# Kernel tuning notes

Measured on AMD Instinct MI355X. Metric: run time of the kernel, lower is better.

Reference implementation:

```python
import jax, jax.numpy as jnp
import numpy as np
import math

B, T, D, H = 4, 2048, 1024, 16
HD = D // H  # head dim = 64

def setup_inputs() -> dict:
    key = jax.random.key(0)
    ks = jax.random.split(key, 4)
    scale = 1.0 / math.sqrt(D)
    return {
        "x": jax.random.normal(ks[0], (B, T, D), dtype=jnp.float32),
        "Wq": jax.random.normal(ks[1], (D, D), dtype=jnp.float32) * scale,
        "bq": jnp.zeros((D,), dtype=jnp.float32),
        "Wk": jax.random.normal(ks[2], (D, D), dtype=jnp.float32) * scale,
        "bk": jnp.zeros((D,), dtype=jnp.float32),
        "Wv": jax.random.normal(ks[3], (D, D), dtype=jnp.float32) * scale,
        "bv": jnp.zeros((D,), dtype=jnp.float32),
    }

def reference(x, Wq, bq, Wk, bk, Wv, bv):
    b, t, d = x.shape
    # QKV projections (nn.Dense): x @ W + b
    q = x @ Wq + bq
    k = x @ Wk + bk
    v = x @ Wv + bv
    # b n (h d) -> b h n d
    def split_heads(y):
        return y.reshape(b, t, H, HD).transpose(0, 2, 1, 3)
    q, k, v = split_heads(q), split_heads(k), split_heads(v)
    # scaled dot-product attention; scale by sqrt(features // heads)
    scores = jnp.einsum("bhqd,bhkd->bhqk", q, k) / math.sqrt(HD)
    attn = jax.nn.softmax(scores, axis=-1)
    # dropout rate 0.0 / eval mode => identity
    out = jnp.einsum("bhqk,bhkd->bhqd", attn, v)
    # b h n d -> b n (h d)
    return out.transpose(0, 2, 1, 3).reshape(b, t, d)
```

## Files before the change

### kernel.cpp

```cpp
#include <hip/hip_runtime.h>
#include <math.h>

typedef unsigned short u16;
typedef short short8 __attribute__((ext_vector_type(8)));
typedef u16 u16x4 __attribute__((ext_vector_type(4)));
typedef float f32x4 __attribute__((ext_vector_type(4)));
typedef __bf16 bf16x8 __attribute__((ext_vector_type(8)));

#define B_ 4
#define T_ 2048
#define D_ 1024
#define H_ 16
#define HD_ 64
#define BT_ 8192

__device__ __forceinline__ u16 f2bf(float f) {
  unsigned u = __builtin_bit_cast(unsigned, f);
  u = u + 0x7fffu + ((u >> 16) & 1u);
  return (u16)(u >> 16);
}
__device__ __forceinline__ f32x4 mfma16(short8 a, short8 b, f32x4 c) {
  return __builtin_amdgcn_mfma_f32_16x16x32_bf16(
      __builtin_bit_cast(bf16x8, a), __builtin_bit_cast(bf16x8, b), c, 0, 0, 0);
}
__device__ __forceinline__ void async16(u16* lds, const u16* g) {
  __builtin_amdgcn_global_load_lds(
      (const __attribute__((address_space(1))) unsigned int*)g,
      (__attribute__((address_space(3))) unsigned int*)lds, 16, 0, 0);
}

__global__ __launch_bounds__(256) void prep(
    const float* __restrict__ x, const float* __restrict__ Wq,
    const float* __restrict__ Wk, const float* __restrict__ Wv,
    u16* __restrict__ xbf, u16* __restrict__ wtq, u16* __restrict__ wtk,
    u16* __restrict__ wtv) {
  __shared__ float sh[32][33];
  if (blockIdx.y < 256) {
    int bid = blockIdx.y * 32 + blockIdx.x;
    int i = (bid * 256 + threadIdx.x) * 4;
    float4 v = *(const float4*)&x[i];
    u16x4 o = {f2bf(v.x), f2bf(v.y), f2bf(v.z), f2bf(v.w)};
    *(u16x4*)&xbf[i] = o;
    return;
  }
  const int yy = blockIdx.y - 256;
  const int wsel = yy >> 5;
  const float* in = (wsel == 0) ? Wq : (wsel == 1) ? Wk : Wv;
  u16* out = (wsel == 0) ? wtq : (wsel == 1) ? wtk : wtv;
  const int bx = blockIdx.x * 32, by = (yy & 31) * 32;
  const int col = threadIdx.x & 31, r8 = threadIdx.x >> 5;
#pragma unroll
  for (int i = 0; i < 4; i++) {
    int row = r8 + i * 8;
    sh[row][col] = in[(size_t)(by + row) * 1024 + bx + col];
  }
  __syncthreads();
#pragma unroll
  for (int i = 0; i < 4; i++) {
    int row = r8 + i * 8;
    out[(size_t)(bx + row) * 1024 + by + col] = f2bf(sh[col][row]);
  }
}

__global__ __launch_bounds__(512, 2) void gemm_qkv3(
    const u16* __restrict__ xbf, const u16* __restrict__ wtq,
    const u16* __restrict__ wtk, const u16* __restrict__ wtv,
    const float* __restrict__ bq, const float* __restrict__ bk,
    const float* __restrict__ bv, u16* __restrict__ qh, u16* __restrict__ kh,
    u16* __restrict__ vth, float qscale) {
  extern __shared__ __align__(16) u16 smem[];
  u16* As = smem;
  u16* Bs = smem + 32768;

  const int proj = blockIdx.y >> 2;
  const int fy = blockIdx.y & 3;
  const u16* Rm;
  const u16* Cm;
  const float* bias;
  u16* out;
  float scale;
  int r0, c0, vmode;
  if (proj == 0) {
    Rm = wtq; Cm = xbf; bias = bq; out = qh; scale = qscale; vmode = 0;
    r0 = fy * 256; c0 = blockIdx.x * 256;
  } else if (proj == 1) {
    Rm = wtk; Cm = xbf; bias = bk; out = kh; scale = 1.0f; vmode = 0;
    r0 = fy * 256; c0 = blockIdx.x * 256;
  } else {
    Rm = xbf; Cm = wtv; bias = bv; out = vth; scale = 1.0f; vmode = 1;
    r0 = blockIdx.x * 256; c0 = fy * 256;
  }
  const int tid = threadIdx.x;
  const int lane = tid & 63;
  const int w = tid >> 6;
  const int wr = w >> 2, wc = w & 3;
  const int c = lane & 15, q4 = lane >> 4;
  const int cx7 = c & 7;
  const int sr = tid >> 3, pc = tid & 7;
  const int scx = (pc ^ (sr & 7)) * 8;
  const int k0o = (q4 ^ cx7) * 8;
  const int k1o = ((4 + q4) ^ cx7) * 8;
  const int brow0 = (wc & 1) * 64;

  f32x4 acc[8][4];
#pragma unroll
  for (int i = 0; i < 8; i++)
#pragma unroll
    for (int j = 0; j < 4; j++) {
      f32x4 z = {0.f, 0.f, 0.f, 0.f};
      acc[i][j] = z;
    }

#define STAGE_A(n, h)                                                        \
  {                                                                          \
    const u16* s_ = Rm + (size_t)(r0 + (h)*128 + sr) * 1024 + (n)*64 + scx;  \
    u16* d_ = As + ((((n)&1) * 2 + (h)) * 8192) + tid * 8;                   \
    async16(d_, s_);                                                         \
    async16(d_ + 4096, s_ + (size_t)64 * 1024);                              \
  }
#define STAGE_B(n, h)                                                        \
  {                                                                          \
    const u16* s_ = Cm + (size_t)(c0 + (h)*128 + sr) * 1024 + (n)*64 + scx;  \
    u16* d_ = Bs + ((((n)&1) * 2 + (h)) * 8192) + tid * 8;                   \
    async16(d_, s_);                                                         \
    async16(d_ + 4096, s_ + (size_t)64 * 1024);                              \
  }

  STAGE_B(0, 0); STAGE_A(0, 0); STAGE_B(0, 1); STAGE_A(0, 1);
  STAGE_B(1, 0); STAGE_A(1, 0);
  asm volatile("s_waitcnt vmcnt(4)" ::: "memory");
  asm volatile("s_barrier" ::: "memory");

#pragma unroll 2
  for (int n = 0; n < 16; ++n) {
    const u16* Aslot = As + (((n & 1) * 2 + wr) * 8192);
    const u16* Bslot = Bs + (((n & 1) * 2 + (wc >> 1)) * 8192);
    short8 aF[4][2], bF[4][2];

#pragma unroll
    for (int ii = 0; ii < 4; ii++) {
      aF[ii][0] = *(const short8*)&Aslot[(ii * 16 + c) * 64 + k0o];
      aF[ii][1] = *(const short8*)&Aslot[(ii * 16 + c) * 64 + k1o];
    }
#pragma unroll
    for (int jj = 0; jj < 2; jj++) {
      bF[jj][0] = *(const short8*)&Bslot[(brow0 + jj * 16 + c) * 64 + k0o];
      bF[jj][1] = *(const short8*)&Bslot[(brow0 + jj * 16 + c) * 64 + k1o];
    }
    STAGE_B((n + 1) & 15, 1);
    asm volatile("s_barrier" ::: "memory");
    __builtin_amdgcn_s_setprio(1);
#pragma unroll
    for (int ii = 0; ii < 4; ii++)
#pragma unroll
      for (int jj = 0; jj < 2; jj++) {
        acc[ii][jj] = mfma16(aF[ii][0], bF[jj][0], acc[ii][jj]);
        acc[ii][jj] = mfma16(aF[ii][1], bF[jj][1], acc[ii][jj]);
      }
    __builtin_amdgcn_s_setprio(0);
    asm volatile("s_barrier" ::: "memory");

#pragma unroll
    for (int jj = 2; jj < 4; jj++) {
      bF[jj][0] = *(const short8*)&Bslot[(brow0 + jj * 16 + c) * 64 + k0o];
      bF[jj][1] = *(const short8*)&Bslot[(brow0 + jj * 16 + c) * 64 + k1o];
    }
    STAGE_A((n + 1) & 15, 1);
    asm volatile("s_barrier" ::: "memory");
    __builtin_amdgcn_s_setprio(1);
#pragma unroll
    for (int ii = 0; ii < 4; ii++)
#pragma unroll
      for (int jj = 2; jj < 4; jj++) {
        acc[ii][jj] = mfma16(aF[ii][0], bF[jj][0], acc[ii][jj]);
        acc[ii][jj] = mfma16(aF[ii][1], bF[jj][1], acc[ii][jj]);
      }
    __builtin_amdgcn_s_setprio(0);
    asm volatile("s_barrier" ::: "memory");

#pragma unroll
    for (int ii = 0; ii < 4; ii++) {
      aF[ii][0] = *(const short8*)&Aslot[((4 + ii) * 16 + c) * 64 + k0o];
      aF[ii][1] = *(const short8*)&Aslot[((4 + ii) * 16 + c) * 64 + k1o];
    }
    STAGE_B((n + 2) & 15, 0);
    asm volatile("s_barrier" ::: "memory");
    __builtin_amdgcn_s_setprio(1);
#pragma unroll
    for (int ii = 0; ii < 4; ii++)
#pragma unroll
      for (int jj = 0; jj < 2; jj++) {
        acc[4 + ii][jj] = mfma16(aF[ii][0], bF[jj][0], acc[4 + ii][jj]);
        acc[4 + ii][jj] = mfma16(aF[ii][1], bF[jj][1], acc[4 + ii][jj]);
      }
    __builtin_amdgcn_s_setprio(0);
    asm volatile("s_barrier" ::: "memory");

    STAGE_A((n + 2) & 15, 0);
    asm volatile("s_barrier" ::: "memory");
    __builtin_amdgcn_s_setprio(1);
#pragma unroll
    for (int ii = 0; ii < 4; ii++)
#pragma unroll
      for (int jj = 2; jj < 4; jj++) {
        acc[4 + ii][jj] = mfma16(aF[ii][0], bF[jj][0], acc[4 + ii][jj]);
        acc[4 + ii][jj] = mfma16(aF[ii][1], bF[jj][1], acc[4 + ii][jj]);
      }
    __builtin_amdgcn_s_setprio(0);
    asm volatile("s_waitcnt vmcnt(4)" ::: "memory");
    asm volatile("s_barrier" ::: "memory");
  }
#undef STAGE_A
#undef STAGE_B

  if (vmode == 0) {
#pragma unroll
    for (int mi = 0; mi < 8; mi++) {
      int ng = r0 + wr * 128 + mi * 16 + q4 * 4;
      int h = ng >> 6, hd = ng & 63;
#pragma unroll
      for (int ni = 0; ni < 4; ni++) {
        int tg = c0 + wc * 64 + ni * 16 + c;
        int b = tg >> 11, tt = tg & 2047;
        u16x4 o;
#pragma unroll
        for (int r = 0; r < 4; r++)
          o[r] = f2bf((acc[mi][ni][r] + bias[ng + r]) * scale);
        *(u16x4*)&out[(((size_t)(b * 16 + h) * 2048 + tt) << 6) + hd] = o;
      }
    }
  } else {
#pragma unroll
    for (int mi = 0; mi < 8; mi++) {
      int tg = r0 + wr * 128 + mi * 16 + q4 * 4;
      int b = tg >> 11, tt = tg & 2047;
      int tp = (tt & ~63) | (((tt >> 2) & 3) << 4) | (((tt >> 4) & 3) << 2);
#pragma unroll
      for (int ni = 0; ni < 4; ni++) {
        int ng = c0 + wc * 64 + ni * 16 + c;
        int h = ng >> 6, hd = ng & 63;
        float bb = bias[ng];
        u16x4 o;
#pragma unroll
        for (int r = 0; r < 4; r++) o[r] = f2bf(acc[mi][ni][r] + bb);
        *(u16x4*)&out[((size_t)((b * 16 + h) * 64 + hd)) * 2048 + tp] = o;
      }
    }
  }
}

__global__ __launch_bounds__(256, 2) void attn_fused(const u16* __restrict__ Qh,
                                                     const u16* __restrict__ Kh,
                                                     const u16* __restrict__ VTh,
                                                     float* __restrict__ out) {
  __shared__ __align__(16) u16 Ks[2][64 * 64];
  __shared__ __align__(16) u16 VTs[2][64 * 64];
  const int tid = threadIdx.x;
  const int w = tid >> 6, lane = tid & 63;
  const int c = lane & 15, q4 = lane >> 4;
  const int cx7 = c & 7;
  const int qt = blockIdx.x, bh = blockIdx.y;

  short8 qf[4][2];
#pragma unroll
  for (int nblk = 0; nblk < 4; nblk++) {
    const u16* Qp =
        Qh + ((size_t)bh * T_ + qt * 256 + w * 64 + nblk * 16 + c) * 64;
    qf[nblk][0] = *(const short8*)&Qp[q4 * 8];
    qf[nblk][1] = *(const short8*)&Qp[32 + q4 * 8];
  }

  const u16* Kb = Kh + (size_t)bh * T_ * 64;
  const u16* Vb = VTh + (size_t)bh * 64 * T_;

  f32x4 O[4][4];
#pragma unroll
  for (int nblk = 0; nblk < 4; nblk++)
#pragma unroll
    for (int nb = 0; nb < 4; nb++) {
      f32x4 z = {0.f, 0.f, 0.f, 0.f};
      O[nblk][nb] = z;
    }
  float lsum[4] = {0.f, 0.f, 0.f, 0.f};

  const int sr = tid >> 3, pc = tid & 7;

#pragma unroll
  for (int i = 0; i < 2; i++) {
    int r = i * 32 + sr;
    int sc = (pc ^ (r & 7)) * 8;
    async16(&Ks[0][(i * 256 + tid) * 8], &Kb[(size_t)r * 64 + sc]);
    async16(&VTs[0][(i * 256 + tid) * 8], &Vb[(size_t)r * T_ + sc]);
  }

  for (int it = 0; it < T_ / 64; it++) {
    const int cur = it & 1;
    __syncthreads();
    if (it + 1 < T_ / 64) {
      const int kt = (it + 1) * 64;
#pragma unroll
      for (int i = 0; i < 2; i++) {
        int r = i * 32 + sr;
        int sc = (pc ^ (r & 7)) * 8;
        async16(&Ks[cur ^ 1][(i * 256 + tid) * 8],
                &Kb[(size_t)(kt + r) * 64 + sc]);
        async16(&VTs[cur ^ 1][(i * 256 + tid) * 8],
                &Vb[(size_t)r * T_ + kt + sc]);
      }
    }

#pragma unroll
    for (int p = 0; p < 2; p++) {
      f32x4 S[2][4];
#pragma unroll
      for (int kbi = 0; kbi < 2; kbi++) {
        const int kb = p * 2 + kbi;
        short8 k0 =
            *(const short8*)&Ks[cur][(kb * 16 + c) * 64 + ((q4 ^ cx7) * 8)];
        short8 k1 = *(const short8*)&Ks[cur][(kb * 16 + c) * 64 +
                                             (((4 + q4) ^ cx7) * 8)];
#pragma unroll
        for (int nblk = 0; nblk < 4; nblk++) {
          f32x4 z = {0.f, 0.f, 0.f, 0.f};
          S[kbi][nblk] = mfma16(k0, qf[nblk][0], z);
          S[kbi][nblk] = mfma16(k1, qf[nblk][1], S[kbi][nblk]);
        }
      }

      short8 pf8[4];
#pragma unroll
      for (int nblk = 0; nblk < 4; nblk++) {
        float e[8];
#pragma unroll
        for (int kbi = 0; kbi < 2; kbi++)
#pragma unroll
          for (int r = 0; r < 4; r++)
            e[kbi * 4 + r] = __builtin_amdgcn_exp2f(S[kbi][nblk][r]);
        lsum[nblk] += ((e[0] + e[1]) + (e[2] + e[3])) +
                      ((e[4] + e[5]) + (e[6] + e[7]));
        bf16x8 t = {(__bf16)e[0], (__bf16)e[1], (__bf16)e[2], (__bf16)e[3],
                    (__bf16)e[4], (__bf16)e[5], (__bf16)e[6], (__bf16)e[7]};
        pf8[nblk] = __builtin_bit_cast(short8, t);
      }

#pragma unroll
      for (int nb = 0; nb < 4; nb++) {
        short8 vf = *(const short8*)&VTs[cur][(nb * 16 + c) * 64 +
                                              (((q4 * 2 + p) ^ cx7) * 8)];
#pragma unroll
        for (int nblk = 0; nblk < 4; nblk++)
          O[nblk][nb] = mfma16(pf8[nblk], vf, O[nblk][nb]);
      }
    }
  }

#pragma unroll
  for (int nblk = 0; nblk < 4; nblk++) {
    lsum[nblk] += __shfl_xor(lsum[nblk], 16);
    lsum[nblk] += __shfl_xor(lsum[nblk], 32);
  }

  const int bq = bh >> 4, h = bh & 15;
#pragma unroll
  for (int nblk = 0; nblk < 4; nblk++)
#pragma unroll
    for (int r = 0; r < 4; r++) {
      float rl = 1.0f / __shfl(lsum[nblk], q4 * 4 + r);
      int t = qt * 256 + w * 64 + nblk * 16 + q4 * 4 + r;
#pragma unroll
      for (int nb = 0; nb < 4; nb++)
        out[((size_t)(bq * T_ + t)) * 1024 + h * 64 + nb * 16 + c] =
            O[nblk][nb][r] * rl;
    }
}

extern "C" void kernel_launch(void* const* d_in, const int* in_sizes, int n_in,
                              void* d_out, int out_size, void* d_ws, size_t ws_size,
                              hipStream_t stream) {
  (void)in_sizes; (void)n_in; (void)out_size; (void)ws_size;
  const float* x  = (const float*)d_in[0];
  const float* Wq = (const float*)d_in[1];
  const float* bq = (const float*)d_in[2];
  const float* Wk = (const float*)d_in[3];
  const float* bk = (const float*)d_in[4];
  const float* Wv = (const float*)d_in[5];
  const float* bv = (const float*)d_in[6];
  float* out = (float*)d_out;

  u16* ob  = (u16*)d_out;
  u16* xbf = ob;
  u16* wtq = ob + (size_t)BT_ * D_;
  u16* wtk = wtq + (size_t)D_ * D_;
  u16* wtv = wtk + (size_t)D_ * D_;

  u16* ws  = (u16*)d_ws;
  u16* qh  = ws;
  u16* kh  = qh + (size_t)BT_ * D_;
  u16* vth = kh + (size_t)BT_ * D_;

  prep<<<dim3(32, 352), 256, 0, stream>>>(x, Wq, Wk, Wv, xbf, wtq, wtk, wtv);

  const float qscale = 0.125f * 1.44269504088896f;
  gemm_qkv3<<<dim3(32, 12), 512, 131072, stream>>>(xbf, wtq, wtk, wtv, bq, bk,
                                                   bv, qh, kh, vth, qscale);

  attn_fused<<<dim3(8, 64), 256, 0, stream>>>(qh, kh, vth, out);
}
```

Measured before the change: 225.0 us.

## Shrink QKV GEMM tile to 128x256 and restructure pipeline stages

The QKV projection GEMM moves from 256x256 output tiles to 128x256 tiles, so the grid grows from 384 to 768 blocks. The A-operand staging becomes a single 128-row slot per stage. The inner loop drops from four MFMA phases to two, with fewer barriers and a wait count adjusted to match. LDS use falls from 128 KB to 96 KB, and the accumulators shrink from 8x4 to 4x4 per wave. The aim is better CU occupancy and load balance across the larger grid, at the cost of lower operand reuse per block and more global traffic for the B operand.

```diff
diff --git a/kernel.cpp b/kernel.cpp
--- a/kernel.cpp
+++ b/kernel.cpp
@@ -70,10 +70,10 @@
     u16* __restrict__ vth, float qscale) {
   extern __shared__ __align__(16) u16 smem[];
   u16* As = smem;
-  u16* Bs = smem + 32768;
-
-  const int proj = blockIdx.y >> 2;
-  const int fy = blockIdx.y & 3;
+  u16* Bs = smem + 16384;
+
+  const int proj = blockIdx.y;
+  const int bx = blockIdx.x;
   const u16* Rm;
   const u16* Cm;
   const float* bias;
@@ -82,13 +82,13 @@
   int r0, c0, vmode;
   if (proj == 0) {
     Rm = wtq; Cm = xbf; bias = bq; out = qh; scale = qscale; vmode = 0;
-    r0 = fy * 256; c0 = blockIdx.x * 256;
+    r0 = (bx & 7) * 128; c0 = (bx >> 3) * 256;
   } else if (proj == 1) {
     Rm = wtk; Cm = xbf; bias = bk; out = kh; scale = 1.0f; vmode = 0;
-    r0 = fy * 256; c0 = blockIdx.x * 256;
+    r0 = (bx & 7) * 128; c0 = (bx >> 3) * 256;
   } else {
     Rm = xbf; Cm = wtv; bias = bv; out = vth; scale = 1.0f; vmode = 1;
-    r0 = blockIdx.x * 256; c0 = fy * 256;
+    r0 = (bx >> 2) * 128; c0 = (bx & 3) * 256;
   }
   const int tid = threadIdx.x;
   const int lane = tid & 63;
@@ -100,60 +100,62 @@
   const int scx = (pc ^ (sr & 7)) * 8;
   const int k0o = (q4 ^ cx7) * 8;
   const int k1o = ((4 + q4) ^ cx7) * 8;
+  const int arow0 = wr * 64;
   const int brow0 = (wc & 1) * 64;
 
-  f32x4 acc[8][4];
-#pragma unroll
-  for (int i = 0; i < 8; i++)
+  f32x4 acc[4][4];
+#pragma unroll
+  for (int i = 0; i < 4; i++)
 #pragma unroll
     for (int j = 0; j < 4; j++) {
       f32x4 z = {0.f, 0.f, 0.f, 0.f};
       acc[i][j] = z;
     }
 
-#define STAGE_A(n, h)                                                        \
-  {                                                                          \
-    const u16* s_ = Rm + (size_t)(r0 + (h)*128 + sr) * 1024 + (n)*64 + scx;  \
-    u16* d_ = As + ((((n)&1) * 2 + (h)) * 8192) + tid * 8;                   \
-    async16(d_, s_);                                                         \
-    async16(d_ + 4096, s_ + (size_t)64 * 1024);                              \
-  }
-#define STAGE_B(n, h)                                                        \
-  {                                                                          \
-    const u16* s_ = Cm + (size_t)(c0 + (h)*128 + sr) * 1024 + (n)*64 + scx;  \
-    u16* d_ = Bs + ((((n)&1) * 2 + (h)) * 8192) + tid * 8;                   \
-    async16(d_, s_);                                                         \
-    async16(d_ + 4096, s_ + (size_t)64 * 1024);                              \
-  }
-
-  STAGE_B(0, 0); STAGE_A(0, 0); STAGE_B(0, 1); STAGE_A(0, 1);
-  STAGE_B(1, 0); STAGE_A(1, 0);
-  asm volatile("s_waitcnt vmcnt(4)" ::: "memory");
+#define STAGE_A(n)                                                          \
+  {                                                                         \
+    const u16* s_ = Rm + (size_t)(r0 + sr) * 1024 + (n)*64 + scx;           \
+    u16* d_ = As + ((n)&1) * 8192 + tid * 8;                                \
+    async16(d_, s_);                                                        \
+    async16(d_ + 4096, s_ + (size_t)64 * 1024);                             \
+  }
+#define STAGE_B(n, h)                                                       \
+  {                                                                         \
+    const u16* s_ = Cm + (size_t)(c0 + (h)*128 + sr) * 1024 + (n)*64 + scx; \
+    u16* d_ = Bs + ((((n)&1) * 2 + (h)) * 8192) + tid * 8;                  \
+    async16(d_, s_);                                                        \
+    async16(d_ + 4096, s_ + (size_t)64 * 1024);                             \
+  }
+
+  STAGE_A(0); STAGE_B(0, 0); STAGE_B(0, 1);
+  STAGE_B(1, 0);
+  asm volatile("s_waitcnt vmcnt(2)" ::: "memory");
   asm volatile("s_barrier" ::: "memory");
 
 #pragma unroll 2
   for (int n = 0; n < 16; ++n) {
-    const u16* Aslot = As + (((n & 1) * 2 + wr) * 8192);
+    const u16* Aslot = As + (n & 1) * 8192;
     const u16* Bslot = Bs + (((n & 1) * 2 + (wc >> 1)) * 8192);
-    short8 aF[4][2], bF[4][2];
-
-#pragma unroll
-    for (int ii = 0; ii < 4; ii++) {
-      aF[ii][0] = *(const short8*)&Aslot[(ii * 16 + c) * 64 + k0o];
-      aF[ii][1] = *(const short8*)&Aslot[(ii * 16 + c) * 64 + k1o];
-    }
-#pragma unroll
-    for (int jj = 0; jj < 2; jj++) {
+    short8 aF[2][2], bF[4][2];
+
+#pragma unroll
+    for (int ii = 0; ii < 2; ii++) {
+      aF[ii][0] = *(const short8*)&Aslot[(arow0 + ii * 16 + c) * 64 + k0o];
+      aF[ii][1] = *(const short8*)&Aslot[(arow0 + ii * 16 + c) * 64 + k1o];
+    }
+#pragma unroll
+    for (int jj = 0; jj < 4; jj++) {
       bF[jj][0] = *(const short8*)&Bslot[(brow0 + jj * 16 + c) * 64 + k0o];
       bF[jj][1] = *(const short8*)&Bslot[(brow0 + jj * 16 + c) * 64 + k1o];
     }
     STAGE_B((n + 1) & 15, 1);
+    STAGE_A((n + 1) & 15);
     asm volatile("s_barrier" ::: "memory");
     __builtin_amdgcn_s_setprio(1);
 #pragma unroll
-    for (int ii = 0; ii < 4; ii++)
-#pragma unroll
-      for (int jj = 0; jj < 2; jj++) {
+    for (int ii = 0; ii < 2; ii++)
+#pragma unroll
+      for (int jj = 0; jj < 4; jj++) {
         acc[ii][jj] = mfma16(aF[ii][0], bF[jj][0], acc[ii][jj]);
         acc[ii][jj] = mfma16(aF[ii][1], bF[jj][1], acc[ii][jj]);
       }
@@ -161,53 +163,22 @@
     asm volatile("s_barrier" ::: "memory");
 
 #pragma unroll
-    for (int jj = 2; jj < 4; jj++) {
-      bF[jj][0] = *(const short8*)&Bslot[(brow0 + jj * 16 + c) * 64 + k0o];
-      bF[jj][1] = *(const short8*)&Bslot[(brow0 + jj * 16 + c) * 64 + k1o];
-    }
-    STAGE_A((n + 1) & 15, 1);
-    asm volatile("s_barrier" ::: "memory");
-    __builtin_amdgcn_s_setprio(1);
-#pragma unroll
-    for (int ii = 0; ii < 4; ii++)
-#pragma unroll
-      for (int jj = 2; jj < 4; jj++) {
-        acc[ii][jj] = mfma16(aF[ii][0], bF[jj][0], acc[ii][jj]);
-        acc[ii][jj] = mfma16(aF[ii][1], bF[jj][1], acc[ii][jj]);
-      }
-    __builtin_amdgcn_s_setprio(0);
-    asm volatile("s_barrier" ::: "memory");
-
-#pragma unroll
-    for (int ii = 0; ii < 4; ii++) {
-      aF[ii][0] = *(const short8*)&Aslot[((4 + ii) * 16 + c) * 64 + k0o];
-      aF[ii][1] = *(const short8*)&Aslot[((4 + ii) * 16 + c) * 64 + k1o];
+    for (int ii = 0; ii < 2; ii++) {
+      aF[ii][0] = *(const short8*)&Aslot[(arow0 + (2 + ii) * 16 + c) * 64 + k0o];
+      aF[ii][1] = *(const short8*)&Aslot[(arow0 + (2 + ii) * 16 + c) * 64 + k1o];
     }
     STAGE_B((n + 2) & 15, 0);
     asm volatile("s_barrier" ::: "memory");
     __builtin_amdgcn_s_setprio(1);
 #pragma unroll
-    for (int ii = 0; ii < 4; ii++)
-#pragma unroll
-      for (int jj = 0; jj < 2; jj++) {
-        acc[4 + ii][jj] = mfma16(aF[ii][0], bF[jj][0], acc[4 + ii][jj]);
-        acc[4 + ii][jj] = mfma16(aF[ii][1], bF[jj][1], acc[4 + ii][jj]);
+    for (int ii = 0; ii < 2; ii++)
+#pragma unroll
+      for (int jj = 0; jj < 4; jj++) {
+        acc[2 + ii][jj] = mfma16(aF[ii][0], bF[jj][0], acc[2 + ii][jj]);
+        acc[2 + ii][jj] = mfma16(aF[ii][1], bF[jj][1], acc[2 + ii][jj]);
       }
     __builtin_amdgcn_s_setprio(0);
-    asm volatile("s_barrier" ::: "memory");
-
-    STAGE_A((n + 2) & 15, 0);
-    asm volatile("s_barrier" ::: "memory");
-    __builtin_amdgcn_s_setprio(1);
-#pragma unroll
-    for (int ii = 0; ii < 4; ii++)
-#pragma unroll
-      for (int jj = 2; jj < 4; jj++) {
-        acc[4 + ii][jj] = mfma16(aF[ii][0], bF[jj][0], acc[4 + ii][jj]);
-        acc[4 + ii][jj] = mfma16(aF[ii][1], bF[jj][1], acc[4 + ii][jj]);
-      }
-    __builtin_amdgcn_s_setprio(0);
-    asm volatile("s_waitcnt vmcnt(4)" ::: "memory");
+    asm volatile("s_waitcnt vmcnt(2)" ::: "memory");
     asm volatile("s_barrier" ::: "memory");
   }
 #undef STAGE_A
@@ -215,8 +186,8 @@
 
   if (vmode == 0) {
 #pragma unroll
-    for (int mi = 0; mi < 8; mi++) {
-      int ng = r0 + wr * 128 + mi * 16 + q4 * 4;
+    for (int mi = 0; mi < 4; mi++) {
+      int ng = r0 + wr * 64 + mi * 16 + q4 * 4;
       int h = ng >> 6, hd = ng & 63;
 #pragma unroll
       for (int ni = 0; ni < 4; ni++) {
@@ -231,8 +202,8 @@
     }
   } else {
 #pragma unroll
-    for (int mi = 0; mi < 8; mi++) {
-      int tg = r0 + wr * 128 + mi * 16 + q4 * 4;
+    for (int mi = 0; mi < 4; mi++) {
+      int tg = r0 + wr * 64 + mi * 16 + q4 * 4;
       int b = tg >> 11, tt = tg & 2047;
       int tp = (tt & ~63) | (((tt >> 2) & 3) << 4) | (((tt >> 4) & 3) << 2);
 #pragma unroll
@@ -401,8 +372,8 @@
   prep<<<dim3(32, 352), 256, 0, stream>>>(x, Wq, Wk, Wv, xbf, wtq, wtk, wtv);
 
   const float qscale = 0.125f * 1.44269504088896f;
-  gemm_qkv3<<<dim3(32, 12), 512, 131072, stream>>>(xbf, wtq, wtk, wtv, bq, bk,
-                                                   bv, qh, kh, vth, qscale);
+  gemm_qkv3<<<dim3(256, 3), 512, 98304, stream>>>(xbf, wtq, wtk, wtv, bq, bk,
+                                                  bv, qh, kh, vth, qscale);
 
   attn_fused<<<dim3(8, 64), 256, 0, stream>>>(qh, kh, vth, out);
 }
```

Result: slower. 239.9 us (+6.6%).

## Load K and V fragments directly from global memory, removing LDS staging

Applied to the files above, without the earlier changes.

The attention kernel no longer double-buffers K and V^T tiles in shared memory with async copies and barriers. Each wave now reads its MFMA operand fragments straight from global memory, relying on L1/L2 caching, and the loop is unrolled by two. This removes LDS traffic and __syncthreads per tile. In exchange, the four waves fetch the same K/V data redundantly, and global-load latency is exposed directly in the inner loop.

```diff
diff --git a/kernel.cpp b/kernel.cpp
--- a/kernel.cpp
+++ b/kernel.cpp
@@ -253,12 +253,9 @@
                                                      const u16* __restrict__ Kh,
                                                      const u16* __restrict__ VTh,
                                                      float* __restrict__ out) {
-  __shared__ __align__(16) u16 Ks[2][64 * 64];
-  __shared__ __align__(16) u16 VTs[2][64 * 64];
   const int tid = threadIdx.x;
   const int w = tid >> 6, lane = tid & 63;
   const int c = lane & 15, q4 = lane >> 4;
-  const int cx7 = c & 7;
   const int qt = blockIdx.x, bh = blockIdx.y;
 
   short8 qf[4][2];
@@ -270,8 +267,8 @@
     qf[nblk][1] = *(const short8*)&Qp[32 + q4 * 8];
   }
 
-  const u16* Kb = Kh + (size_t)bh * T_ * 64;
-  const u16* Vb = VTh + (size_t)bh * 64 * T_;
+  const u16* Kp = Kh + (size_t)bh * T_ * 64 + (size_t)c * 64 + q4 * 8;
+  const u16* Vp = VTh + (size_t)bh * 64 * T_ + (size_t)c * T_;
 
   f32x4 O[4][4];
 #pragma unroll
@@ -283,31 +280,9 @@
     }
   float lsum[4] = {0.f, 0.f, 0.f, 0.f};
 
-  const int sr = tid >> 3, pc = tid & 7;
-
-#pragma unroll
-  for (int i = 0; i < 2; i++) {
-    int r = i * 32 + sr;
-    int sc = (pc ^ (r & 7)) * 8;
-    async16(&Ks[0][(i * 256 + tid) * 8], &Kb[(size_t)r * 64 + sc]);
-    async16(&VTs[0][(i * 256 + tid) * 8], &Vb[(size_t)r * T_ + sc]);
-  }
-
+#pragma unroll 2
   for (int it = 0; it < T_ / 64; it++) {
-    const int cur = it & 1;
-    __syncthreads();
-    if (it + 1 < T_ / 64) {
-      const int kt = (it + 1) * 64;
-#pragma unroll
-      for (int i = 0; i < 2; i++) {
-        int r = i * 32 + sr;
-        int sc = (pc ^ (r & 7)) * 8;
-        async16(&Ks[cur ^ 1][(i * 256 + tid) * 8],
-                &Kb[(size_t)(kt + r) * 64 + sc]);
-        async16(&VTs[cur ^ 1][(i * 256 + tid) * 8],
-                &Vb[(size_t)r * T_ + kt + sc]);
-      }
-    }
+    const int kt = it * 64;
 
 #pragma unroll
     for (int p = 0; p < 2; p++) {
@@ -315,10 +290,9 @@
 #pragma unroll
       for (int kbi = 0; kbi < 2; kbi++) {
         const int kb = p * 2 + kbi;
-        short8 k0 =
-            *(const short8*)&Ks[cur][(kb * 16 + c) * 64 + ((q4 ^ cx7) * 8)];
-        short8 k1 = *(const short8*)&Ks[cur][(kb * 16 + c) * 64 +
-                                             (((4 + q4) ^ cx7) * 8)];
+        const u16* kp = Kp + (size_t)(kt + kb * 16) * 64;
+        short8 k0 = *(const short8*)kp;
+        short8 k1 = *(const short8*)(kp + 32);
 #pragma unroll
         for (int nblk = 0; nblk < 4; nblk++) {
           f32x4 z = {0.f, 0.f, 0.f, 0.f};
@@ -345,8 +319,8 @@
 
 #pragma unroll
       for (int nb = 0; nb < 4; nb++) {
-        short8 vf = *(const short8*)&VTs[cur][(nb * 16 + c) * 64 +
-                                              (((q4 * 2 + p) ^ cx7) * 8)];
+        short8 vf = *(const short8*)&Vp[(size_t)(nb * 16) * T_ + kt +
+                                        (q4 * 2 + p) * 8];
 #pragma unroll
         for (int nblk = 0; nblk < 4; nblk++)
           O[nblk][nb] = mfma16(pf8[nblk], vf, O[nblk][nb]);
```

Measured after the change: 287.2 us. +27.6%, slower.
